# Kernel tuning notes

Hardware: AMD Instinct MI355X
Metric: run time of the kernel (lower is better)

Reference implementation:

```python
import jax, jax.numpy as jnp
import numpy as np

B, NF, S, L, H, MID, KS, NC, DENSE = 16, 8, 16, 256, 128, 32, 8, 10, 512
COEFF = 0.1
BN_EPS = 1e-5


def _normalize(x):
    return x / jnp.maximum(jnp.linalg.norm(x, axis=-1, keepdims=True), 1e-12)


def _sparsemax(z):
    # sparsemax over last axis (Martins & Astudillo 2016)
    zs = jnp.flip(jnp.sort(z, axis=-1), axis=-1)
    k = jnp.arange(1, z.shape[-1] + 1, dtype=z.dtype)
    cum = jnp.cumsum(zs, axis=-1)
    support = (1.0 + k * zs) > cum
    ksup = jnp.sum(support, axis=-1, keepdims=True)
    tau = (jnp.take_along_axis(cum, ksup - 1, axis=-1) - 1.0) / ksup.astype(z.dtype)
    return jnp.maximum(z - tau, 0.0)


def _bn_ncl(x, g, b, m, v):  # eval-mode BatchNorm1d on [N, C, L]
    return g[None, :, None] * (x - m[None, :, None]) * jax.lax.rsqrt(v[None, :, None] + BN_EPS) + b[None, :, None]


def _bn_nc(x, g, b, m, v):  # eval-mode BatchNorm1d on [N, C]
    return g * (x - m) * jax.lax.rsqrt(v + BN_EPS) + b


def _conv(x, w, pad):
    return jax.lax.conv_general_dilated(x, w, (1,), [(pad, pad)], dimension_numbers=('NCH', 'OIH', 'NCH'))


def _maxpool2(x):  # MaxPool1d(kernel=2, stride=2, padding=1): -inf padded
    return jax.lax.reduce_window(x, -jnp.inf, jax.lax.max, (1, 1, 2), (1, 1, 2), ((0, 0), (0, 0), (1, 1)))


def _cnn(x, cw1, bn1, cw2, bn2, cw3, bn3):
    x = _maxpool2(jax.nn.relu(_bn_ncl(_conv(x, cw1, KS // 2), *bn1)))
    x = _maxpool2(jax.nn.relu(_bn_ncl(_conv(x, cw2, 4), *bn2)))
    x = _maxpool2(jax.nn.relu(_bn_ncl(_conv(x, cw3, 4), *bn3)))
    return jnp.mean(x, axis=-1)  # AdaptiveAvgPool1d(1) -> [N, H]


def _alpha_beta(x, cw1, bn1, cw2, bn2, cw3, bn3, Wq, bq, Wk, bk, Wv, bv):
    b = x.shape[0]
    xf = jnp.transpose(x, (1, 0, 2, 3)).reshape(NF, b * S, 1, L)
    rep = jax.vmap(_cnn)(xf, cw1, bn1, cw2, bn2, cw3, bn3)  # [F, B*S, H]
    rep = rep.reshape(NF, b, S, H)
    Q = jax.nn.elu(rep @ Wq + bq)
    K = jax.nn.leaky_relu(rep @ Wk + bk)
    V = jax.nn.leaky_relu(rep @ Wv + bv)
    # mean_t(Q @ K^T) == Q @ mean_t(K); then scale by sqrt(d_k)
    scores = jnp.einsum('fbsh,fbh->fbs', Q, jnp.mean(K, axis=2)) / jnp.sqrt(jnp.float32(H))
    intra_aw = _sparsemax(scores)                             # [F, B, S]
    Z = _normalize(jnp.einsum('fbs,fbsh->fbh', intra_aw, V))  # [F, B, H]
    Kn = _normalize(rep)
    inter_scores = jnp.einsum('ibh,fbsh->ifbs', Z, Kn)        # cosine scores (Z already unit-norm)
    inter_aw = _sparsemax(inter_scores)                       # [I, F, B, S]
    U = jnp.einsum('ifbs,fbsh->ibh', inter_aw, rep) / NF      # mean over feature axis f
    Hc = _normalize(jnp.concatenate([Z, U], axis=-1))         # [F, B, 2H]
    feat = jnp.transpose(Hc, (1, 0, 2)).reshape(b, NF * 2 * H)
    return feat, intra_aw, inter_aw


def _forward(src_x, src_y, tgt_x, cw1, bn1_g, bn1_b, bn1_m, bn1_v, cw2, bn2_g, bn2_b, bn2_m, bn2_v, cw3, bn3_g, bn3_b, bn3_m, bn3_v, Wq, bq, Wk, bk, Wv, bv, bnc1_g, bnc1_b, bnc1_m, bnc1_v, W1, b1, bnc2_g, bnc2_b, bnc2_m, bnc2_v, W2, b2):
    bn1 = (bn1_g, bn1_b, bn1_m, bn1_v)
    bn2 = (bn2_g, bn2_b, bn2_m, bn2_v)
    bn3 = (bn3_g, bn3_b, bn3_m, bn3_v)
    sf, sa, sb = _alpha_beta(src_x, cw1, bn1, cw2, bn2, cw3, bn3, Wq, bq, Wk, bk, Wv, bv)
    _, ta, tb = _alpha_beta(tgt_x, cw1, bn1, cw2, bn2, cw3, bn3, Wq, bq, Wk, bk, Wv, bv)
    h = _bn_nc(sf, bnc1_g, bnc1_b, bnc1_m, bnc1_v) @ W1 + b1
    h = jax.nn.leaky_relu(_bn_nc(h, bnc2_g, bnc2_b, bnc2_m, bnc2_v))
    y_pred = jax.nn.softmax(h @ W2 + b2, axis=-1)
    # MMD domain losses (detached in original via torch.tensor(list))
    da = jnp.mean(sa - ta, axis=-2)                           # [F, S]
    loss_a = COEFF * jnp.mean(jnp.linalg.norm(da, axis=-1))
    db = jnp.mean(sb - tb, axis=-2)                           # [I, F, S]
    loss_b = COEFF * jnp.mean(jnp.sqrt(jnp.sum(db * db, axis=(1, 2))))
    dom = jax.lax.stop_gradient(loss_a + loss_b)
    # CrossEntropyLoss applied to already-softmaxed preds, as in source
    logp = jax.nn.log_softmax(y_pred, axis=-1)
    ce = -jnp.mean(logp[jnp.arange(y_pred.shape[0]), src_y])
    return y_pred, ce + dom


def setup_inputs() -> dict:
    ks = jax.random.split(jax.random.key(0), 40)
    rn = lambda i, sh, s=1.0: s * jax.random.normal(ks[i], sh, dtype=jnp.float32)
    ru = lambda i, sh, lo, hi: jax.random.uniform(ks[i], sh, jnp.float32, lo, hi)
    return {
        'src_x': rn(0, (B, NF, S, L)),
        'src_y': jax.random.randint(ks[1], (B,), 0, NC),
        'tgt_x': rn(2, (B, NF, S, L)),
        'cw1': rn(3, (NF, MID, 1, KS), 0.1),
        'bn1_g': ru(4, (NF, MID), 0.75, 1.25), 'bn1_b': rn(5, (NF, MID), 0.1),
        'bn1_m': rn(6, (NF, MID), 0.1), 'bn1_v': ru(7, (NF, MID), 0.5, 1.5),
        'cw2': rn(8, (NF, 2 * MID, MID, 8), 0.05),
        'bn2_g': ru(9, (NF, 2 * MID), 0.75, 1.25), 'bn2_b': rn(10, (NF, 2 * MID), 0.1),
        'bn2_m': rn(11, (NF, 2 * MID), 0.1), 'bn2_v': ru(12, (NF, 2 * MID), 0.5, 1.5),
        'cw3': rn(13, (NF, H, 2 * MID, 8), 0.05),
        'bn3_g': ru(14, (NF, H), 0.75, 1.25), 'bn3_b': rn(15, (NF, H), 0.1),
        'bn3_m': rn(16, (NF, H), 0.1), 'bn3_v': ru(17, (NF, H), 0.5, 1.5),
        'Wq': rn(18, (H, H), 0.05), 'bq': rn(19, (H,), 0.02),
        'Wk': rn(20, (H, H), 0.05), 'bk': rn(21, (H,), 0.02),
        'Wv': rn(22, (H, H), 0.05), 'bv': rn(23, (H,), 0.02),
        'bnc1_g': ru(24, (NF * 2 * H,), 0.75, 1.25), 'bnc1_b': rn(25, (NF * 2 * H,), 0.1),
        'bnc1_m': rn(26, (NF * 2 * H,), 0.1), 'bnc1_v': ru(27, (NF * 2 * H,), 0.5, 1.5),
        'W1': rn(28, (NF * 2 * H, DENSE), 0.03), 'b1': rn(29, (DENSE,), 0.02),
        'bnc2_g': ru(30, (DENSE,), 0.75, 1.25), 'bnc2_b': rn(31, (DENSE,), 0.1),
        'bnc2_m': rn(32, (DENSE,), 0.1), 'bnc2_v': ru(33, (DENSE,), 0.5, 1.5),
        'W2': rn(34, (DENSE, NC), 0.05), 'b2': rn(35, (NC,), 0.02),
    }


def reference(src_x, src_y, tgt_x, cw1, bn1_g, bn1_b, bn1_m, bn1_v, cw2, bn2_g, bn2_b, bn2_m, bn2_v, cw3, bn3_g, bn3_b, bn3_m, bn3_v, Wq, bq, Wk, bk, Wv, bv, bnc1_g, bnc1_b, bnc1_m, bnc1_v, W1, b1, bnc2_g, bnc2_b, bnc2_m, bnc2_v, W2, b2):
    return _forward(src_x, src_y, tgt_x, cw1, bn1_g, bn1_b, bn1_m, bn1_v, cw2, bn2_g, bn2_b, bn2_m, bn2_v, cw3, bn3_g, bn3_b, bn3_m, bn3_v, Wq, bq, Wk, bk, Wv, bv, bnc1_g, bnc1_b, bnc1_m, bnc1_v, W1, b1, bnc2_g, bnc2_b, bnc2_m, bnc2_v, W2, b2)
```

## Files before the change

### kernel.cpp

```cpp
#include <hip/hip_runtime.h>

typedef unsigned short u16;
typedef unsigned int u32;
typedef __attribute__((ext_vector_type(8))) short bfrag;
typedef __attribute__((ext_vector_type(4))) float ffrag;

__device__ __forceinline__ float lrelu(float x) { return x >= 0.f ? x : 0.01f * x; }
__device__ __forceinline__ float eluf(float x)  { return x > 0.f ? x : expm1f(x); }
__device__ __forceinline__ u16 f2bf(float f) {
    u32 x = __float_as_uint(f);
    return (u16)((x + 0x7fffu + ((x >> 16) & 1u)) >> 16);
}
__device__ __forceinline__ u16 f2bt(float f) {
    return (u16)(__float_as_uint(f) >> 16);
}
__device__ __forceinline__ float bf2f(u16 u) {
    return __uint_as_float(((u32)u) << 16);
}

__device__ void sparsemax16(const float* z, float* out) {
    float zs[16];
    for (int i = 0; i < 16; ++i) zs[i] = z[i];
    for (int i = 1; i < 16; ++i) {
        float key = zs[i]; int j = i - 1;
        while (j >= 0 && zs[j] < key) { zs[j + 1] = zs[j]; --j; }
        zs[j + 1] = key;
    }
    float cum[16];
    cum[0] = zs[0];
    for (int i = 1; i < 16; ++i) cum[i] = cum[i - 1] + zs[i];
    int ksup = 0;
    for (int k = 1; k <= 16; ++k)
        if (1.0f + (float)k * zs[k - 1] > cum[k - 1]) ksup++;
    if (ksup < 1) ksup = 1;
    float tau = (cum[ksup - 1] - 1.0f) / (float)ksup;
    for (int i = 0; i < 16; ++i) out[i] = fmaxf(z[i] - tau, 0.0f);
}

__global__ __launch_bounds__(256) void k_wprep(
    const float* __restrict__ w2, const float* __restrict__ w3,
    const float* __restrict__ Wq, const float* __restrict__ Wk,
    const float* __restrict__ Wv,
    u16* __restrict__ wpk2, u16* __restrict__ wpk3, u16* __restrict__ wqkv)
{
    int i = blockIdx.x * 256 + threadIdx.x;
    if (i < 131072) {
        int j = i & 7, L = (i >> 3) & 63, kc = (i >> 9) & 7, nt = (i >> 12) & 3, f = i >> 14;
        int co = nt * 16 + (L & 15);
        int ci = ((L >> 4) << 3) + j;
        wpk2[i] = f2bf(w2[(((size_t)f * 64 + co) * 32 + ci) * 8 + kc]);
    } else if (i < 131072 + 524288) {
        int i2 = i - 131072;
        int j = i2 & 7, L = (i2 >> 3) & 63, kc = (i2 >> 9) & 15, nt = (i2 >> 13) & 7, f = i2 >> 16;
        int co = nt * 16 + (L & 15);
        int ci = ((kc & 1) << 5) + ((L >> 4) << 3) + j;
        wpk3[i2] = f2bf(w3[(((size_t)f * 128 + co) * 64 + ci) * 8 + (kc >> 1)]);
    } else if (i < 131072 + 524288 + 49152) {
        int j2 = i - 655360;
        int proj = j2 >> 14, idx = j2 & 16383;
        int jj = idx & 7, L = (idx >> 3) & 63, kc = (idx >> 9) & 3, nt = idx >> 11;
        int n = nt * 16 + (L & 15);
        int k = kc * 32 + ((L >> 4) << 3) + jj;
        const float* W = proj == 0 ? Wq : (proj == 1 ? Wk : Wv);
        wqkv[j2] = f2bf(W[k * 128 + n]);
    }
}

#define S1T_STRIDE 40
#define S2T_STRIDE 72
#define RB2_STRIDE 68
#define RB3_STRIDE 140
#define RB_OFF 6336
#define SMEM_U16 (RB_OFF + 67 * RB3_STRIDE)

__global__ __launch_bounds__(256) void k_cnn(
    const float* __restrict__ xs, const float* __restrict__ xt,
    const float* __restrict__ w1, const float* __restrict__ g1, const float* __restrict__ b1,
    const float* __restrict__ m1, const float* __restrict__ v1,
    const float* __restrict__ g2, const float* __restrict__ b2,
    const float* __restrict__ m2, const float* __restrict__ v2,
    const float* __restrict__ g3, const float* __restrict__ b3,
    const float* __restrict__ m3, const float* __restrict__ v3,
    const u16* __restrict__ wpk2, const u16* __restrict__ wpk3,
    float* __restrict__ rep)
{
    __shared__ __align__(16) u16 smem[SMEM_U16];
    float* xin = (float*)(smem + RB_OFF);

    int tid = threadIdx.x, blk = blockIdx.x;
    int pass = blk >> 11, f = (blk >> 8) & 7, n = blk & 255;
    int bb = n >> 4, ss = n & 15;
    int lane = tid & 63, w = tid >> 6;
    const float* x = pass ? xt : xs;
    float* rep_p = rep + (size_t)pass * 262144;

    {
        u32* z = (u32*)smem;
        for (int i = tid; i < 3168; i += 256) z[i] = 0;
        for (int i = tid; i < 264; i += 256) xin[i] = 0.f;
    }
    __syncthreads();
    {
        const float* xr = x + (((size_t)bb * 8 + f) * 16 + ss) * 256;
        for (int i = tid; i < 256; i += 256) xin[i + 4] = xr[i];
    }
    __syncthreads();

    if (tid < 208) {
        int cc = tid & 7, jc = tid >> 3;
        int co0 = cc * 4, j0 = jc * 5;
        float wr[4][8];
        for (int c = 0; c < 4; ++c) {
            const float4* q = reinterpret_cast<const float4*>(w1 + ((size_t)f * 32 + co0 + c) * 8);
            float4 a = q[0], bq = q[1];
            wr[c][0] = a.x; wr[c][1] = a.y; wr[c][2] = a.z; wr[c][3] = a.w;
            wr[c][4] = bq.x; wr[c][5] = bq.y; wr[c][6] = bq.z; wr[c][7] = bq.w;
        }
        int px[10];
        for (int i = 0; i < 10; ++i) {
            int p = 2 * j0 - 1 + i;
            px[i] = p < 0 ? 0 : (p > 256 ? 256 : p);
        }
        float acc[4][10];
        for (int c = 0; c < 4; ++c) for (int i = 0; i < 10; ++i) acc[c][i] = 0.f;
        for (int k = 0; k < 8; ++k) {
            float xv[10];
            for (int i = 0; i < 10; ++i) xv[i] = xin[px[i] + k];
            for (int c = 0; c < 4; ++c)
                for (int i = 0; i < 10; ++i) acc[c][i] += wr[c][k] * xv[i];
        }
        for (int c = 0; c < 4; ++c) {
            int co = co0 + c;
            float sc = g1[f * 32 + co] * rsqrtf(v1[f * 32 + co] + 1e-5f);
            float sh = b1[f * 32 + co] - m1[f * 32 + co] * sc;
            for (int jj = 0; jj < 5; ++jj) {
                int j = j0 + jj;
                if (j < 129) {
                    float a0 = fmaxf(acc[c][2 * jj] * sc + sh, 0.f);
                    float a1 = fmaxf(acc[c][2 * jj + 1] * sc + sh, 0.f);
                    smem[(j + 4) * S1T_STRIDE + co] = f2bt(fmaxf(a0, a1));
                }
            }
        }
    }
    __syncthreads();

    {
        int nt = w;
        bfrag B2[8];
        const bfrag* gB = reinterpret_cast<const bfrag*>(wpk2);
        for (int kc = 0; kc < 8; ++kc)
            B2[kc] = gB[(((size_t)f * 4 + nt) * 8 + kc) * 64 + lane];
        int co = nt * 16 + (lane & 15);
        float sc = g2[f * 64 + co] * rsqrtf(v2[f * 64 + co] + 1e-5f);
        float sh = b2[f * 64 + co] - m2[f * 64 + co] * sc;
        int arow = lane & 15, ci0 = (lane >> 4) << 3;
        for (int mt = 0; mt < 9; ++mt) {
            ffrag C = {0.f, 0.f, 0.f, 0.f};
            int rb = mt * 16 + arow;
            for (int kc = 0; kc < 8; ++kc) {
                bfrag A = *reinterpret_cast<const bfrag*>(&smem[(rb + kc) * S1T_STRIDE + ci0]);
                C = __builtin_amdgcn_mfma_f32_16x16x32_bf16(A, B2[kc], C, 0, 0, 0);
            }
            int p0 = mt * 16 + ((lane >> 4) << 2);
            for (int r = 0; r < 4; ++r) {
                int p = p0 + r;
                if (p < 130)
                    smem[RB_OFF + p * RB2_STRIDE + co] = f2bt(fmaxf(C[r] * sc + sh, 0.f));
            }
        }
    }
    __syncthreads();

    {
        u32* z = (u32*)smem;
        for (int i = tid; i < 3168; i += 256) z[i] = 0;
    }
    __syncthreads();

    for (int e = tid; e < 66 * 64; e += 256) {
        int j = e >> 6, ci = e & 63;
        float vmax;
        if (j == 0) {
            vmax = bf2f(smem[RB_OFF + 0 * RB2_STRIDE + ci]);
        } else if (j == 65) {
            vmax = bf2f(smem[RB_OFF + 129 * RB2_STRIDE + ci]);
        } else {
            float a0 = bf2f(smem[RB_OFF + (2 * j - 1) * RB2_STRIDE + ci]);
            float a1 = bf2f(smem[RB_OFF + (2 * j) * RB2_STRIDE + ci]);
            vmax = fmaxf(a0, a1);
        }
        smem[(j + 4) * S2T_STRIDE + ci] = f2bt(vmax);
    }
    __syncthreads();

    for (int t = 0; t < 2; ++t) {
        int nt = w * 2 + t;
        bfrag B3[16];
        const bfrag* gB = reinterpret_cast<const bfrag*>(wpk3);
        for (int kc = 0; kc < 16; ++kc)
            B3[kc] = gB[(((size_t)f * 8 + nt) * 16 + kc) * 64 + lane];
        int co = nt * 16 + (lane & 15);
        float sc = g3[f * 128 + co] * rsqrtf(v3[f * 128 + co] + 1e-5f);
        float sh = b3[f * 128 + co] - m3[f * 128 + co] * sc;
        int arow = lane & 15, q8 = (lane >> 4) << 3;
        for (int mt = 0; mt < 5; ++mt) {
            ffrag C = {0.f, 0.f, 0.f, 0.f};
            int rb = mt * 16 + arow;
            for (int kc = 0; kc < 16; ++kc) {
                int row = rb + (kc >> 1);
                int ci0 = ((kc & 1) << 5) + q8;
                bfrag A = *reinterpret_cast<const bfrag*>(&smem[row * S2T_STRIDE + ci0]);
                C = __builtin_amdgcn_mfma_f32_16x16x32_bf16(A, B3[kc], C, 0, 0, 0);
            }
            int p0 = mt * 16 + ((lane >> 4) << 2);
            for (int r = 0; r < 4; ++r) {
                int p = p0 + r;
                if (p < 67)
                    smem[RB_OFF + p * RB3_STRIDE + co] = f2bt(fmaxf(C[r] * sc + sh, 0.f));
            }
        }
    }
    __syncthreads();

    if (tid < 128) {
        int co = tid;
        float sum = bf2f(smem[RB_OFF + 0 * RB3_STRIDE + co]);
        for (int j = 1; j < 34; ++j) {
            float a0 = bf2f(smem[RB_OFF + (2 * j - 1) * RB3_STRIDE + co]);
            float a1 = bf2f(smem[RB_OFF + (2 * j) * RB3_STRIDE + co]);
            sum += fmaxf(a0, a1);
        }
        rep_p[(((size_t)f * 256) + n) * 128 + co] = sum * (1.0f / 34.0f);
    }
}

__global__ __launch_bounds__(256) void k_attn1(
    const float* __restrict__ rep, const u16* __restrict__ wqkv,
    const float* __restrict__ bq, const float* __restrict__ bk,
    const float* __restrict__ bv,
    float* __restrict__ Zn, float* __restrict__ rninv, float* __restrict__ iaw)
{
    __shared__ __align__(16) u16 repbf[16 * 136];
    __shared__ float KmL[128], ZL[128], awL[16], scoresL[16], r2L[16];
    __shared__ float spart[4][4][4];
    __shared__ float redL[4];
    int tid = threadIdx.x;
    int pass = blockIdx.x >> 7, f = (blockIdx.x >> 4) & 7, b = blockIdx.x & 15;
    const float* rp = rep + (size_t)pass * 262144 + ((size_t)f * 256 + b * 16) * 128;
    float* Zn_p = Zn + (size_t)pass * 16384;
    float* rninv_p = rninv + (size_t)pass * 2048;
    float* iaw_p = iaw + (size_t)pass * 2048;

    {
        int s = tid >> 4, i = tid & 15, h0 = i * 8;
        const float4* q4 = reinterpret_cast<const float4*>(rp + s * 128 + h0);
        float4 a = q4[0], c = q4[1];
        float p2 = a.x*a.x + a.y*a.y + a.z*a.z + a.w*a.w
                 + c.x*c.x + c.y*c.y + c.z*c.z + c.w*c.w;
        bfrag pk;
        pk[0] = (short)f2bt(a.x); pk[1] = (short)f2bt(a.y);
        pk[2] = (short)f2bt(a.z); pk[3] = (short)f2bt(a.w);
        pk[4] = (short)f2bt(c.x); pk[5] = (short)f2bt(c.y);
        pk[6] = (short)f2bt(c.z); pk[7] = (short)f2bt(c.w);
        *reinterpret_cast<bfrag*>(&repbf[s * 136 + h0]) = pk;
        p2 += __shfl_xor(p2, 1); p2 += __shfl_xor(p2, 2);
        p2 += __shfl_xor(p2, 4); p2 += __shfl_xor(p2, 8);
        if (i == 0) r2L[s] = p2;
    }
    __syncthreads();

    int lane = tid & 63, w = tid >> 6, arow = lane & 15, q = lane >> 4;
    bfrag A[4];
    for (int kc = 0; kc < 4; ++kc)
        A[kc] = *reinterpret_cast<const bfrag*>(&repbf[arow * 136 + kc * 32 + q * 8]);

    float qv[2][4], vvv[2][4];
    int colv[2];
    const bfrag* BB = reinterpret_cast<const bfrag*>(wqkv);
    for (int t = 0; t < 2; ++t) {
        int nt = w * 2 + t;
        ffrag cq = {0.f,0.f,0.f,0.f}, ck = {0.f,0.f,0.f,0.f}, cv = {0.f,0.f,0.f,0.f};
        for (int kc = 0; kc < 4; ++kc) {
            int fi = (nt * 4 + kc) * 64 + lane;
            bfrag Bq = BB[fi];
            bfrag Bk = BB[2048 + fi];
            bfrag Bv = BB[4096 + fi];
            cq = __builtin_amdgcn_mfma_f32_16x16x32_bf16(A[kc], Bq, cq, 0, 0, 0);
            ck = __builtin_amdgcn_mfma_f32_16x16x32_bf16(A[kc], Bk, ck, 0, 0, 0);
            cv = __builtin_amdgcn_mfma_f32_16x16x32_bf16(A[kc], Bv, cv, 0, 0, 0);
        }
        int col = nt * 16 + arow;
        colv[t] = col;
        float bqc = bq[col], bkc = bk[col], bvc = bv[col];
        float kpt = 0.f;
        for (int r = 0; r < 4; ++r) {
            qv[t][r] = eluf(cq[r] + bqc);
            vvv[t][r] = lrelu(cv[r] + bvc);
            kpt += lrelu(ck[r] + bkc);
        }
        kpt += __shfl_xor(kpt, 16);
        kpt += __shfl_xor(kpt, 32);
        if (q == 0) KmL[col] = kpt * (1.f / 16.f);
    }
    __syncthreads();

    {
        float km0 = KmL[colv[0]], km1 = KmL[colv[1]];
        float ps[4];
        for (int r = 0; r < 4; ++r) {
            float v = qv[0][r] * km0 + qv[1][r] * km1;
            v += __shfl_xor(v, 1); v += __shfl_xor(v, 2);
            v += __shfl_xor(v, 4); v += __shfl_xor(v, 8);
            ps[r] = v;
        }
        if (arow == 0)
            for (int r = 0; r < 4; ++r) spart[w][q][r] = ps[r];
    }
    __syncthreads();
    if (tid < 16) {
        int qq = tid >> 2, rr = tid & 3;
        float sc = spart[0][qq][rr] + spart[1][qq][rr] + spart[2][qq][rr] + spart[3][qq][rr];
        scoresL[tid] = sc * 0.08838834764831845f;
        rninv_p[f * 256 + b * 16 + tid] = 1.f / fmaxf(sqrtf(r2L[tid]), 1e-12f);
    }
    __syncthreads();
    if (tid == 0) sparsemax16(scoresL, awL);
    __syncthreads();
    if (tid < 16) iaw_p[f * 256 + b * 16 + tid] = awL[tid];

    for (int t = 0; t < 2; ++t) {
        float zp = 0.f;
        for (int r = 0; r < 4; ++r) zp += awL[q * 4 + r] * vvv[t][r];
        zp += __shfl_xor(zp, 16);
        zp += __shfl_xor(zp, 32);
        if (q == 0) ZL[colv[t]] = zp;
    }
    __syncthreads();
    if (tid < 128) {
        float z = ZL[tid];
        float v = z * z;
        v += __shfl_xor(v, 1); v += __shfl_xor(v, 2); v += __shfl_xor(v, 4);
        v += __shfl_xor(v, 8); v += __shfl_xor(v, 16); v += __shfl_xor(v, 32);
        if (lane == 0) redL[w] = v;
    }
    __syncthreads();
    if (tid == 0) redL[2] = 1.f / fmaxf(sqrtf(redL[0] + redL[1]), 1e-12f);
    __syncthreads();
    if (tid < 128)
        Zn_p[((size_t)f * 16 + b) * 128 + tid] = ZL[tid] * redL[2];
}

__global__ __launch_bounds__(256) void k_attn2(
    const float* __restrict__ rep, const float* __restrict__ Zn,
    const float* __restrict__ rninv, float* __restrict__ ibw,
    const float* __restrict__ g, const float* __restrict__ bb,
    const float* __restrict__ mm, const float* __restrict__ vv,
    float* __restrict__ featbn)
{
    __shared__ float ZnL[1024], sc[1024], UL[1024], nrm[8];
    int tid = threadIdx.x;
    int pass = blockIdx.x >> 4, b = blockIdx.x & 15;
    const float* rep_p = rep + (size_t)pass * 262144;
    const float* Zn_p = Zn + (size_t)pass * 16384;
    const float* rninv_p = rninv + (size_t)pass * 2048;
    float* ibw_p = ibw + (size_t)pass * 16384;

    for (int i = tid; i < 1024; i += 256) {
        int ii = i >> 7, h = i & 127;
        ZnL[i] = Zn_p[((size_t)ii * 16 + b) * 128 + h];
    }
    if (tid < 8) nrm[tid] = 0.f;
    __syncthreads();

    for (int e = tid; e < 1024; e += 256) {
        int i = e >> 7, f = (e >> 4) & 7, s = e & 15;
        const float* rr = rep_p + ((size_t)f * 256 + b * 16 + s) * 128;
        float a = 0.f;
        for (int h = 0; h < 128; ++h) a += ZnL[i * 128 + h] * rr[h];
        sc[(i * 8 + f) * 16 + s] = a * rninv_p[f * 256 + b * 16 + s];
    }
    __syncthreads();
    if (tid < 64) {
        int i = tid >> 3, f = tid & 7;
        float aw[16];
        sparsemax16(&sc[(i * 8 + f) * 16], aw);
        for (int s = 0; s < 16; ++s) {
            sc[(i * 8 + f) * 16 + s] = aw[s];
            ibw_p[(((size_t)i * 8 + f) * 16 + b) * 16 + s] = aw[s];
        }
    }
    __syncthreads();
    if (pass == 0) {
        for (int e = tid; e < 1024; e += 256) {
            int i = e >> 7, h = e & 127;
            float u = 0.f;
            for (int f = 0; f < 8; ++f) {
                const float* rr = rep_p + ((size_t)f * 256 + b * 16) * 128 + h;
                const float* aa = &sc[(i * 8 + f) * 16];
                for (int s = 0; s < 16; ++s) u += aa[s] * rr[s * 128];
            }
            UL[e] = u * 0.125f;
        }
        __syncthreads();
        for (int e = tid; e < 1024; e += 256) {
            int f = e >> 7;
            float zz = ZnL[e], uu = UL[e];
            atomicAdd(&nrm[f], zz * zz + uu * uu);
        }
        __syncthreads();
        for (int e = tid; e < 2048; e += 256) {
            int f = e >> 8, d = e & 255;
            float inv = 1.f / fmaxf(sqrtf(nrm[f]), 1e-12f);
            float val = (d < 128 ? ZnL[f * 128 + d] : UL[f * 128 + d - 128]) * inv;
            float scv = g[e] * rsqrtf(vv[e] + 1e-5f);
            featbn[b * 2048 + e] = (val - mm[e]) * scv + bb[e];
        }
    }
}

__global__ __launch_bounds__(256) void k_head1(
    const float* __restrict__ featbn,
    const float* __restrict__ W1, const float* __restrict__ b1,
    const float* __restrict__ g2, const float* __restrict__ bb2,
    const float* __restrict__ mm2, const float* __restrict__ vv2,
    float* __restrict__ h2ws)
{
    __shared__ float featL[2048];
    __shared__ float part[8][32];
    int tid = threadIdx.x, blk = blockIdx.x;
    int b = blk >> 4, cc = blk & 15;
    for (int i = tid; i < 2048; i += 256) featL[i] = featbn[b * 2048 + i];
    __syncthreads();
    int ci = tid & 31, ks = tid >> 5;
    int col = cc * 32 + ci;
    const float* wcol = W1 + (size_t)(ks * 256) * 512 + col;
    const float* fl = featL + ks * 256;
    float a = 0.f;
    for (int c = 0; c < 256; ++c) a += fl[c] * wcol[(size_t)c * 512];
    part[ks][ci] = a;
    __syncthreads();
    if (tid < 32) {
        int colw = cc * 32 + tid;
        float s = b1[colw];
        for (int k2 = 0; k2 < 8; ++k2) s += part[k2][tid];
        float scv = g2[colw] * rsqrtf(vv2[colw] + 1e-5f);
        float val = (s - mm2[colw]) * scv + bb2[colw];
        h2ws[b * 512 + colw] = lrelu(val);
    }
}

__global__ __launch_bounds__(256) void k_tail(
    const float* __restrict__ h2ws,
    const float* __restrict__ W2, const float* __restrict__ b2,
    const float* __restrict__ sa, const float* __restrict__ ta,
    const float* __restrict__ sb, const float* __restrict__ tb,
    const int* __restrict__ sy, float* __restrict__ dout)
{
    __shared__ float h2L[8192];
    __shared__ float lgL[160], ypL[160];
    __shared__ float sA[8], sB[8];
    int tid = threadIdx.x;
    for (int i = tid; i < 8192; i += 256) h2L[i] = h2ws[i];
    if (tid < 8) { sA[tid] = 0.f; sB[tid] = 0.f; }
    __syncthreads();
    if (tid < 160) {
        int b = tid / 10, j = tid - b * 10;
        float a = b2[j];
        const float* h = h2L + b * 512;
        for (int c = 0; c < 512; ++c) a += h[c] * W2[c * 10 + j];
        lgL[tid] = a;
    }
    __syncthreads();
    if (tid < 16) {
        int b = tid;
        float mx = lgL[b * 10];
        for (int j = 1; j < 10; ++j) mx = fmaxf(mx, lgL[b * 10 + j]);
        float sum = 0.f, ex[10];
        for (int j = 0; j < 10; ++j) { ex[j] = expf(lgL[b * 10 + j] - mx); sum += ex[j]; }
        for (int j = 0; j < 10; ++j) {
            float p = ex[j] / sum;
            ypL[b * 10 + j] = p;
            dout[b * 10 + j] = p;
        }
    }
    __syncthreads();
    if (tid < 128) {
        int f = tid >> 4, s = tid & 15;
        float d = 0.f;
        for (int b = 0; b < 16; ++b) d += sa[f * 256 + b * 16 + s] - ta[f * 256 + b * 16 + s];
        d *= (1.f / 16.f);
        atomicAdd(&sA[f], d * d);
    }
    for (int e = tid; e < 1024; e += 256) {
        int i = e >> 7, f = (e >> 4) & 7, s = e & 15;
        float d = 0.f;
        int base = ((i * 8 + f) * 16) * 16 + s;
        for (int b = 0; b < 16; ++b) d += sb[base + b * 16] - tb[base + b * 16];
        d *= (1.f / 16.f);
        atomicAdd(&sB[i], d * d);
    }
    __syncthreads();
    if (tid == 0) {
        float la = 0.f, lb = 0.f;
        for (int f = 0; f < 8; ++f) la += sqrtf(sA[f]);
        for (int i = 0; i < 8; ++i) lb += sqrtf(sB[i]);
        la *= 0.1f / 8.f;
        lb *= 0.1f / 8.f;
        float ce = 0.f;
        for (int b = 0; b < 16; ++b) {
            const float* y = ypL + b * 10;
            float mx = y[0];
            for (int j = 1; j < 10; ++j) mx = fmaxf(mx, y[j]);
            float sum = 0.f;
            for (int j = 0; j < 10; ++j) sum += expf(y[j] - mx);
            float lse = mx + logf(sum);
            ce += lse - y[sy[b]];
        }
        ce *= (1.f / 16.f);
        dout[160] = ce + la + lb;
    }
}

extern "C" void kernel_launch(void* const* d_in, const int* in_sizes, int n_in,
                              void* d_out, int out_size, void* d_ws, size_t ws_size,
                              hipStream_t stream) {
    (void)in_sizes; (void)n_in; (void)out_size; (void)ws_size;
    const float* src_x = (const float*)d_in[0];
    const int*   src_y = (const int*)d_in[1];
    const float* tgt_x = (const float*)d_in[2];
    const float *cw1 = (const float*)d_in[3], *bn1g = (const float*)d_in[4],
                *bn1b = (const float*)d_in[5], *bn1m = (const float*)d_in[6],
                *bn1v = (const float*)d_in[7];
    const float *cw2 = (const float*)d_in[8], *bn2g = (const float*)d_in[9],
                *bn2b = (const float*)d_in[10], *bn2m = (const float*)d_in[11],
                *bn2v = (const float*)d_in[12];
    const float *cw3 = (const float*)d_in[13], *bn3g = (const float*)d_in[14],
                *bn3b = (const float*)d_in[15], *bn3m = (const float*)d_in[16],
                *bn3v = (const float*)d_in[17];
    const float *Wq = (const float*)d_in[18], *bq = (const float*)d_in[19],
                *Wk = (const float*)d_in[20], *bk = (const float*)d_in[21],
                *Wv = (const float*)d_in[22], *bv = (const float*)d_in[23];
    const float *bc1g = (const float*)d_in[24], *bc1b = (const float*)d_in[25],
                *bc1m = (const float*)d_in[26], *bc1v = (const float*)d_in[27];
    const float *W1 = (const float*)d_in[28], *b1 = (const float*)d_in[29];
    const float *bc2g = (const float*)d_in[30], *bc2b = (const float*)d_in[31],
                *bc2m = (const float*)d_in[32], *bc2v = (const float*)d_in[33];
    const float *W2 = (const float*)d_in[34], *b2 = (const float*)d_in[35];

    float* ws = (float*)d_ws;
    size_t o = 0;
    float* rep    = ws + o; o += (size_t)2 * 262144;
    float* Zn     = ws + o; o += (size_t)2 * 16384;
    float* rninv  = ws + o; o += (size_t)2 * 2048;
    float* ia     = ws + o; o += (size_t)2 * 2048;
    float* ib     = ws + o; o += (size_t)2 * 16384;
    float* featbn = ws + o; o += (size_t)16 * 2048;
    float* h2ws   = ws + o; o += (size_t)16 * 512;
    u16* wpk2 = (u16*)(ws + o); o += 65536;
    u16* wpk3 = (u16*)(ws + o); o += 262144;
    u16* wqkv = (u16*)(ws + o); o += 24576;

    k_wprep<<<2752, 256, 0, stream>>>(cw2, cw3, Wq, Wk, Wv, wpk2, wpk3, wqkv);
    k_cnn<<<4096, 256, 0, stream>>>(src_x, tgt_x,
        cw1, bn1g, bn1b, bn1m, bn1v,
        bn2g, bn2b, bn2m, bn2v,
        bn3g, bn3b, bn3m, bn3v,
        wpk2, wpk3, rep);
    k_attn1<<<256, 256, 0, stream>>>(rep, wqkv, bq, bk, bv, Zn, rninv, ia);
    k_attn2<<<32, 256, 0, stream>>>(rep, Zn, rninv, ib, bc1g, bc1b, bc1m, bc1v, featbn);
    k_head1<<<256, 256, 0, stream>>>(featbn, W1, b1, bc2g, bc2b, bc2m, bc2v, h2ws);
    k_tail<<<1, 256, 0, stream>>>(h2ws, W2, b2, ia, ia + 2048, ib, ib + 16384,
                                  src_y, (float*)d_out);
}
```

Before: 333.2 us.

## Fuse attention kernels into one per-batch kernel with rep staged in LDS

Merges k_attn1 and k_attn2 into one kernel of 32 blocks. Each block loads its batch's rep slice (all 8 features) into shared memory once, then computes intra-attention for each feature in a serial loop and goes straight on to inter-attention from LDS. This drops one launch and the global round trips for Zn and rninv, but cuts parallelism from 256 blocks to 32 and uses about 80KB of LDS per block. k_head1 is also reworked to split K into 32 slices with float4 loads of W1 columns.

Result: slower. 405.6 us (+21.8%).

```diff
diff --git a/kernel.cpp b/kernel.cpp
--- a/kernel.cpp
+++ b/kernel.cpp
@@ -235,158 +235,151 @@
     }
 }
 
-__global__ __launch_bounds__(256) void k_attn1(
+__global__ __launch_bounds__(256) void k_attn(
     const float* __restrict__ rep, const u16* __restrict__ wqkv,
     const float* __restrict__ bq, const float* __restrict__ bk,
     const float* __restrict__ bv,
-    float* __restrict__ Zn, float* __restrict__ rninv, float* __restrict__ iaw)
-{
-    __shared__ __align__(16) u16 repbf[16 * 136];
-    __shared__ float KmL[128], ZL[128], awL[16], scoresL[16], r2L[16];
-    __shared__ float spart[4][4][4];
-    __shared__ float redL[4];
-    int tid = threadIdx.x;
-    int pass = blockIdx.x >> 7, f = (blockIdx.x >> 4) & 7, b = blockIdx.x & 15;
-    const float* rp = rep + (size_t)pass * 262144 + ((size_t)f * 256 + b * 16) * 128;
-    float* Zn_p = Zn + (size_t)pass * 16384;
-    float* rninv_p = rninv + (size_t)pass * 2048;
-    float* iaw_p = iaw + (size_t)pass * 2048;
-
-    {
-        int s = tid >> 4, i = tid & 15, h0 = i * 8;
-        const float4* q4 = reinterpret_cast<const float4*>(rp + s * 128 + h0);
-        float4 a = q4[0], c = q4[1];
-        float p2 = a.x*a.x + a.y*a.y + a.z*a.z + a.w*a.w
-                 + c.x*c.x + c.y*c.y + c.z*c.z + c.w*c.w;
-        bfrag pk;
-        pk[0] = (short)f2bt(a.x); pk[1] = (short)f2bt(a.y);
-        pk[2] = (short)f2bt(a.z); pk[3] = (short)f2bt(a.w);
-        pk[4] = (short)f2bt(c.x); pk[5] = (short)f2bt(c.y);
-        pk[6] = (short)f2bt(c.z); pk[7] = (short)f2bt(c.w);
-        *reinterpret_cast<bfrag*>(&repbf[s * 136 + h0]) = pk;
-        p2 += __shfl_xor(p2, 1); p2 += __shfl_xor(p2, 2);
-        p2 += __shfl_xor(p2, 4); p2 += __shfl_xor(p2, 8);
-        if (i == 0) r2L[s] = p2;
-    }
-    __syncthreads();
-
-    int lane = tid & 63, w = tid >> 6, arow = lane & 15, q = lane >> 4;
-    bfrag A[4];
-    for (int kc = 0; kc < 4; ++kc)
-        A[kc] = *reinterpret_cast<const bfrag*>(&repbf[arow * 136 + kc * 32 + q * 8]);
-
-    float qv[2][4], vvv[2][4];
-    int colv[2];
-    const bfrag* BB = reinterpret_cast<const bfrag*>(wqkv);
-    for (int t = 0; t < 2; ++t) {
-        int nt = w * 2 + t;
-        ffrag cq = {0.f,0.f,0.f,0.f}, ck = {0.f,0.f,0.f,0.f}, cv = {0.f,0.f,0.f,0.f};
-        for (int kc = 0; kc < 4; ++kc) {
-            int fi = (nt * 4 + kc) * 64 + lane;
-            bfrag Bq = BB[fi];
-            bfrag Bk = BB[2048 + fi];
-            bfrag Bv = BB[4096 + fi];
-            cq = __builtin_amdgcn_mfma_f32_16x16x32_bf16(A[kc], Bq, cq, 0, 0, 0);
-            ck = __builtin_amdgcn_mfma_f32_16x16x32_bf16(A[kc], Bk, ck, 0, 0, 0);
-            cv = __builtin_amdgcn_mfma_f32_16x16x32_bf16(A[kc], Bv, cv, 0, 0, 0);
-        }
-        int col = nt * 16 + arow;
-        colv[t] = col;
-        float bqc = bq[col], bkc = bk[col], bvc = bv[col];
-        float kpt = 0.f;
-        for (int r = 0; r < 4; ++r) {
-            qv[t][r] = eluf(cq[r] + bqc);
-            vvv[t][r] = lrelu(cv[r] + bvc);
-            kpt += lrelu(ck[r] + bkc);
-        }
-        kpt += __shfl_xor(kpt, 16);
-        kpt += __shfl_xor(kpt, 32);
-        if (q == 0) KmL[col] = kpt * (1.f / 16.f);
-    }
-    __syncthreads();
-
-    {
-        float km0 = KmL[colv[0]], km1 = KmL[colv[1]];
-        float ps[4];
-        for (int r = 0; r < 4; ++r) {
-            float v = qv[0][r] * km0 + qv[1][r] * km1;
-            v += __shfl_xor(v, 1); v += __shfl_xor(v, 2);
-            v += __shfl_xor(v, 4); v += __shfl_xor(v, 8);
-            ps[r] = v;
-        }
-        if (arow == 0)
-            for (int r = 0; r < 4; ++r) spart[w][q][r] = ps[r];
-    }
-    __syncthreads();
-    if (tid < 16) {
-        int qq = tid >> 2, rr = tid & 3;
-        float sc = spart[0][qq][rr] + spart[1][qq][rr] + spart[2][qq][rr] + spart[3][qq][rr];
-        scoresL[tid] = sc * 0.08838834764831845f;
-        rninv_p[f * 256 + b * 16 + tid] = 1.f / fmaxf(sqrtf(r2L[tid]), 1e-12f);
-    }
-    __syncthreads();
-    if (tid == 0) sparsemax16(scoresL, awL);
-    __syncthreads();
-    if (tid < 16) iaw_p[f * 256 + b * 16 + tid] = awL[tid];
-
-    for (int t = 0; t < 2; ++t) {
-        float zp = 0.f;
-        for (int r = 0; r < 4; ++r) zp += awL[q * 4 + r] * vvv[t][r];
-        zp += __shfl_xor(zp, 16);
-        zp += __shfl_xor(zp, 32);
-        if (q == 0) ZL[colv[t]] = zp;
-    }
-    __syncthreads();
-    if (tid < 128) {
-        float z = ZL[tid];
-        float v = z * z;
-        v += __shfl_xor(v, 1); v += __shfl_xor(v, 2); v += __shfl_xor(v, 4);
-        v += __shfl_xor(v, 8); v += __shfl_xor(v, 16); v += __shfl_xor(v, 32);
-        if (lane == 0) redL[w] = v;
-    }
-    __syncthreads();
-    if (tid == 0) redL[2] = 1.f / fmaxf(sqrtf(redL[0] + redL[1]), 1e-12f);
-    __syncthreads();
-    if (tid < 128)
-        Zn_p[((size_t)f * 16 + b) * 128 + tid] = ZL[tid] * redL[2];
-}
-
-__global__ __launch_bounds__(256) void k_attn2(
-    const float* __restrict__ rep, const float* __restrict__ Zn,
-    const float* __restrict__ rninv, float* __restrict__ ibw,
+    float* __restrict__ iaw, float* __restrict__ ibw,
     const float* __restrict__ g, const float* __restrict__ bb,
     const float* __restrict__ mm, const float* __restrict__ vv,
     float* __restrict__ featbn)
 {
-    __shared__ float ZnL[1024], sc[1024], UL[1024], nrm[8];
+    __shared__ float repL[16384];
+    __shared__ __align__(16) u16 repbf[16 * 136];
+    __shared__ float ZnL[1024];
+    __shared__ float scL[1024], UL[1024];
+    __shared__ float rinvL[128], KmL[128], ZL[128];
+    __shared__ float awL[16], scoresL[16];
+    __shared__ float spart[4][4][4], redL[4], nrm[8];
     int tid = threadIdx.x;
     int pass = blockIdx.x >> 4, b = blockIdx.x & 15;
     const float* rep_p = rep + (size_t)pass * 262144;
-    const float* Zn_p = Zn + (size_t)pass * 16384;
-    const float* rninv_p = rninv + (size_t)pass * 2048;
+    float* iaw_p = iaw + (size_t)pass * 2048;
     float* ibw_p = ibw + (size_t)pass * 16384;
-
-    for (int i = tid; i < 1024; i += 256) {
-        int ii = i >> 7, h = i & 127;
-        ZnL[i] = Zn_p[((size_t)ii * 16 + b) * 128 + h];
+    int lane = tid & 63, w = tid >> 6, arow = lane & 15, q = lane >> 4;
+
+    for (int f = 0; f < 8; ++f) {
+        const float4* src = reinterpret_cast<const float4*>(
+            rep_p + ((size_t)f * 256 + b * 16) * 128);
+        float4* dst = reinterpret_cast<float4*>(repL + f * 2048);
+        for (int i = tid; i < 512; i += 256) dst[i] = src[i];
     }
     if (tid < 8) nrm[tid] = 0.f;
     __syncthreads();
+
+    if (tid < 128) {
+        const float* r = repL + tid * 128;
+        float s = 0.f;
+        for (int h = 0; h < 128; ++h) { float v = r[h]; s += v * v; }
+        rinvL[tid] = 1.f / fmaxf(sqrtf(s), 1e-12f);
+    }
+    __syncthreads();
+
+    const bfrag* BB = reinterpret_cast<const bfrag*>(wqkv);
+    for (int f = 0; f < 8; ++f) {
+        {
+            int s = tid >> 4, i = tid & 15, h0 = i * 8;
+            const float* r = repL + (f * 16 + s) * 128 + h0;
+            bfrag pk;
+            for (int j = 0; j < 8; ++j) pk[j] = (short)f2bt(r[j]);
+            *reinterpret_cast<bfrag*>(&repbf[s * 136 + h0]) = pk;
+        }
+        __syncthreads();
+
+        bfrag A[4];
+        for (int kc = 0; kc < 4; ++kc)
+            A[kc] = *reinterpret_cast<const bfrag*>(&repbf[arow * 136 + kc * 32 + q * 8]);
+
+        float qv[2][4], vvv[2][4];
+        int colv[2];
+        for (int t = 0; t < 2; ++t) {
+            int nt = w * 2 + t;
+            ffrag cq = {0.f,0.f,0.f,0.f}, ck = {0.f,0.f,0.f,0.f}, cv = {0.f,0.f,0.f,0.f};
+            for (int kc = 0; kc < 4; ++kc) {
+                int fi = (nt * 4 + kc) * 64 + lane;
+                bfrag Bq = BB[fi];
+                bfrag Bk = BB[2048 + fi];
+                bfrag Bv = BB[4096 + fi];
+                cq = __builtin_amdgcn_mfma_f32_16x16x32_bf16(A[kc], Bq, cq, 0, 0, 0);
+                ck = __builtin_amdgcn_mfma_f32_16x16x32_bf16(A[kc], Bk, ck, 0, 0, 0);
+                cv = __builtin_amdgcn_mfma_f32_16x16x32_bf16(A[kc], Bv, cv, 0, 0, 0);
+            }
+            int col = nt * 16 + arow;
+            colv[t] = col;
+            float bqc = bq[col], bkc = bk[col], bvc = bv[col];
+            float kpt = 0.f;
+            for (int r = 0; r < 4; ++r) {
+                qv[t][r] = eluf(cq[r] + bqc);
+                vvv[t][r] = lrelu(cv[r] + bvc);
+                kpt += lrelu(ck[r] + bkc);
+            }
+            kpt += __shfl_xor(kpt, 16);
+            kpt += __shfl_xor(kpt, 32);
+            if (q == 0) KmL[col] = kpt * (1.f / 16.f);
+        }
+        __syncthreads();
+
+        {
+            float km0 = KmL[colv[0]], km1 = KmL[colv[1]];
+            float ps[4];
+            for (int r = 0; r < 4; ++r) {
+                float v = qv[0][r] * km0 + qv[1][r] * km1;
+                v += __shfl_xor(v, 1); v += __shfl_xor(v, 2);
+                v += __shfl_xor(v, 4); v += __shfl_xor(v, 8);
+                ps[r] = v;
+            }
+            if (arow == 0)
+                for (int r = 0; r < 4; ++r) spart[w][q][r] = ps[r];
+        }
+        __syncthreads();
+        if (tid < 16) {
+            int qq = tid >> 2, rr = tid & 3;
+            float sc = spart[0][qq][rr] + spart[1][qq][rr]
+                     + spart[2][qq][rr] + spart[3][qq][rr];
+            scoresL[tid] = sc * 0.08838834764831845f;
+        }
+        __syncthreads();
+        if (tid == 0) sparsemax16(scoresL, awL);
+        __syncthreads();
+        if (tid < 16) iaw_p[f * 256 + b * 16 + tid] = awL[tid];
+
+        for (int t = 0; t < 2; ++t) {
+            float zp = 0.f;
+            for (int r = 0; r < 4; ++r) zp += awL[q * 4 + r] * vvv[t][r];
+            zp += __shfl_xor(zp, 16);
+            zp += __shfl_xor(zp, 32);
+            if (q == 0) ZL[colv[t]] = zp;
+        }
+        __syncthreads();
+        if (tid < 128) {
+            float z = ZL[tid];
+            float v = z * z;
+            v += __shfl_xor(v, 1); v += __shfl_xor(v, 2); v += __shfl_xor(v, 4);
+            v += __shfl_xor(v, 8); v += __shfl_xor(v, 16); v += __shfl_xor(v, 32);
+            if (lane == 0) redL[w] = v;
+        }
+        __syncthreads();
+        if (tid == 0) redL[2] = 1.f / fmaxf(sqrtf(redL[0] + redL[1]), 1e-12f);
+        __syncthreads();
+        if (tid < 128) ZnL[f * 128 + tid] = ZL[tid] * redL[2];
+        __syncthreads();
+    }
 
     for (int e = tid; e < 1024; e += 256) {
         int i = e >> 7, f = (e >> 4) & 7, s = e & 15;
-        const float* rr = rep_p + ((size_t)f * 256 + b * 16 + s) * 128;
+        const float* zr = ZnL + i * 128;
+        const float* rr = repL + (f * 16 + s) * 128;
         float a = 0.f;
-        for (int h = 0; h < 128; ++h) a += ZnL[i * 128 + h] * rr[h];
-        sc[(i * 8 + f) * 16 + s] = a * rninv_p[f * 256 + b * 16 + s];
+        for (int h = 0; h < 128; ++h) a += zr[h] * rr[h];
+        scL[(i * 8 + f) * 16 + s] = a * rinvL[f * 16 + s];
     }
     __syncthreads();
     if (tid < 64) {
         int i = tid >> 3, f = tid & 7;
         float aw[16];
-        sparsemax16(&sc[(i * 8 + f) * 16], aw);
+        sparsemax16(&scL[(i * 8 + f) * 16], aw);
         for (int s = 0; s < 16; ++s) {
-            sc[(i * 8 + f) * 16 + s] = aw[s];
+            scL[(i * 8 + f) * 16 + s] = aw[s];
             ibw_p[(((size_t)i * 8 + f) * 16 + b) * 16 + s] = aw[s];
         }
     }
@@ -396,8 +389,8 @@
             int i = e >> 7, h = e & 127;
             float u = 0.f;
             for (int f = 0; f < 8; ++f) {
-                const float* rr = rep_p + ((size_t)f * 256 + b * 16) * 128 + h;
-                const float* aa = &sc[(i * 8 + f) * 16];
+                const float* rr = repL + f * 2048 + h;
+                const float* aa = &scL[(i * 8 + f) * 16];
                 for (int s = 0; s < 16; ++s) u += aa[s] * rr[s * 128];
             }
             UL[e] = u * 0.125f;
@@ -427,23 +420,35 @@
     float* __restrict__ h2ws)
 {
     __shared__ float featL[2048];
-    __shared__ float part[8][32];
+    __shared__ float part[32][32];
     int tid = threadIdx.x, blk = blockIdx.x;
     int b = blk >> 4, cc = blk & 15;
-    for (int i = tid; i < 2048; i += 256) featL[i] = featbn[b * 2048 + i];
-    __syncthreads();
-    int ci = tid & 31, ks = tid >> 5;
-    int col = cc * 32 + ci;
-    const float* wcol = W1 + (size_t)(ks * 256) * 512 + col;
-    const float* fl = featL + ks * 256;
-    float a = 0.f;
-    for (int c = 0; c < 256; ++c) a += fl[c] * wcol[(size_t)c * 512];
-    part[ks][ci] = a;
+    {
+        const float4* src = reinterpret_cast<const float4*>(featbn + b * 2048);
+        float4* dst = reinterpret_cast<float4*>(featL);
+        for (int i = tid; i < 512; i += 256) dst[i] = src[i];
+    }
+    __syncthreads();
+    int ks = tid >> 3, cg = tid & 7;
+    int col0 = cc * 32 + cg * 4;
+    float4 acc = {0.f, 0.f, 0.f, 0.f};
+    const float* fl = featL + ks * 64;
+    for (int c = 0; c < 64; ++c) {
+        int k = ks * 64 + c;
+        float4 wv = *reinterpret_cast<const float4*>(W1 + (size_t)k * 512 + col0);
+        float fv = fl[c];
+        acc.x += fv * wv.x; acc.y += fv * wv.y;
+        acc.z += fv * wv.z; acc.w += fv * wv.w;
+    }
+    part[ks][cg * 4 + 0] = acc.x;
+    part[ks][cg * 4 + 1] = acc.y;
+    part[ks][cg * 4 + 2] = acc.z;
+    part[ks][cg * 4 + 3] = acc.w;
     __syncthreads();
     if (tid < 32) {
         int colw = cc * 32 + tid;
         float s = b1[colw];
-        for (int k2 = 0; k2 < 8; ++k2) s += part[k2][tid];
+        for (int k2 = 0; k2 < 32; ++k2) s += part[k2][tid];
         float scv = g2[colw] * rsqrtf(vv2[colw] + 1e-5f);
         float val = (s - mm2[colw]) * scv + bb2[colw];
         h2ws[b * 512 + colw] = lrelu(val);
@@ -551,8 +556,6 @@
     float* ws = (float*)d_ws;
     size_t o = 0;
     float* rep    = ws + o; o += (size_t)2 * 262144;
-    float* Zn     = ws + o; o += (size_t)2 * 16384;
-    float* rninv  = ws + o; o += (size_t)2 * 2048;
     float* ia     = ws + o; o += (size_t)2 * 2048;
     float* ib     = ws + o; o += (size_t)2 * 16384;
     float* featbn = ws + o; o += (size_t)16 * 2048;
@@ -567,8 +570,8 @@
         bn2g, bn2b, bn2m, bn2v,
         bn3g, bn3b, bn3m, bn3v,
         wpk2, wpk3, rep);
-    k_attn1<<<256, 256, 0, stream>>>(rep, wqkv, bq, bk, bv, Zn, rninv, ia);
-    k_attn2<<<32, 256, 0, stream>>>(rep, Zn, rninv, ib, bc1g, bc1b, bc1m, bc1v, featbn);
+    k_attn<<<32, 256, 0, stream>>>(rep, wqkv, bq, bk, bv, ia, ib,
+                                   bc1g, bc1b, bc1m, bc1v, featbn);
     k_head1<<<256, 256, 0, stream>>>(featbn, W1, b1, bc2g, bc2b, bc2m, bc2v, h2ws);
     k_tail<<<1, 256, 0, stream>>>(h2ws, W2, b2, ia, ia + 2048, ib, ib + 16384,
                                   src_y, (float*)d_out);
```

## Split inter-attention kernel across query features and vectorize head matmul

Applied to the files above, without the earlier changes.

k_attn2 now runs 256 blocks instead of 32, one per (pass, batch, query feature). Each block stages the batch's rep slice into shared memory with float4 loads and computes a single query's scores, sparsemax, aggregation and norm using wave shuffles in place of shared atomics. k_head1 has each thread load float4 columns of W1 over a 64-wide K slice with a 32-way partial reduction, which coalesces the weight reads. The cost is that the rep slice is reloaded redundantly by 8 blocks and each block uses 64KB of LDS.

Result: faster. 314.9 us (-5.5%).

```diff
diff --git a/kernel.cpp b/kernel.cpp
--- a/kernel.cpp
+++ b/kernel.cpp
@@ -358,61 +358,66 @@
     const float* __restrict__ mm, const float* __restrict__ vv,
     float* __restrict__ featbn)
 {
-    __shared__ float ZnL[1024], sc[1024], UL[1024], nrm[8];
-    int tid = threadIdx.x;
-    int pass = blockIdx.x >> 4, b = blockIdx.x & 15;
+    __shared__ float repL[16384];
+    __shared__ float ZiL[128], scores[128], UL[128];
+    __shared__ float awLf[8][16];
+    __shared__ float redL[2];
+    int tid = threadIdx.x, blk = blockIdx.x;
+    int pass = blk >> 7, b = (blk >> 3) & 15, i = blk & 7;
     const float* rep_p = rep + (size_t)pass * 262144;
-    const float* Zn_p = Zn + (size_t)pass * 16384;
-    const float* rninv_p = rninv + (size_t)pass * 2048;
-    float* ibw_p = ibw + (size_t)pass * 16384;
-
-    for (int i = tid; i < 1024; i += 256) {
-        int ii = i >> 7, h = i & 127;
-        ZnL[i] = Zn_p[((size_t)ii * 16 + b) * 128 + h];
-    }
-    if (tid < 8) nrm[tid] = 0.f;
-    __syncthreads();
-
-    for (int e = tid; e < 1024; e += 256) {
-        int i = e >> 7, f = (e >> 4) & 7, s = e & 15;
-        const float* rr = rep_p + ((size_t)f * 256 + b * 16 + s) * 128;
+
+    for (int f = 0; f < 8; ++f) {
+        const float4* src = reinterpret_cast<const float4*>(
+            rep_p + ((size_t)f * 256 + b * 16) * 128);
+        float4* dst = reinterpret_cast<float4*>(repL + f * 2048);
+        for (int t = tid; t < 512; t += 256) dst[t] = src[t];
+    }
+    if (tid < 128) ZiL[tid] = Zn[(size_t)pass * 16384 + ((size_t)i * 16 + b) * 128 + tid];
+    __syncthreads();
+
+    if (tid < 128) {
+        int f = tid >> 4, s = tid & 15;
+        const float* rr = repL + tid * 128;
         float a = 0.f;
-        for (int h = 0; h < 128; ++h) a += ZnL[i * 128 + h] * rr[h];
-        sc[(i * 8 + f) * 16 + s] = a * rninv_p[f * 256 + b * 16 + s];
-    }
-    __syncthreads();
-    if (tid < 64) {
-        int i = tid >> 3, f = tid & 7;
+        for (int h = 0; h < 128; ++h) a += ZiL[h] * rr[h];
+        scores[tid] = a * rninv[(size_t)pass * 2048 + f * 256 + b * 16 + s];
+    }
+    __syncthreads();
+    if (tid < 8) {
         float aw[16];
-        sparsemax16(&sc[(i * 8 + f) * 16], aw);
-        for (int s = 0; s < 16; ++s) {
-            sc[(i * 8 + f) * 16 + s] = aw[s];
-            ibw_p[(((size_t)i * 8 + f) * 16 + b) * 16 + s] = aw[s];
-        }
-    }
-    __syncthreads();
+        sparsemax16(&scores[tid * 16], aw);
+        for (int s = 0; s < 16; ++s) awLf[tid][s] = aw[s];
+    }
+    __syncthreads();
+    if (tid < 128) {
+        int f = tid >> 4, s = tid & 15;
+        ibw[(size_t)pass * 16384 + (((size_t)i * 8 + f) * 16 + b) * 16 + s] = awLf[f][s];
+    }
     if (pass == 0) {
-        for (int e = tid; e < 1024; e += 256) {
-            int i = e >> 7, h = e & 127;
+        if (tid < 128) {
+            int h = tid;
             float u = 0.f;
             for (int f = 0; f < 8; ++f) {
-                const float* rr = rep_p + ((size_t)f * 256 + b * 16) * 128 + h;
-                const float* aa = &sc[(i * 8 + f) * 16];
+                const float* rr = repL + f * 2048 + h;
+                const float* aa = awLf[f];
                 for (int s = 0; s < 16; ++s) u += aa[s] * rr[s * 128];
             }
-            UL[e] = u * 0.125f;
+            UL[h] = u * 0.125f;
         }
         __syncthreads();
-        for (int e = tid; e < 1024; e += 256) {
-            int f = e >> 7;
-            float zz = ZnL[e], uu = UL[e];
-            atomicAdd(&nrm[f], zz * zz + uu * uu);
+        if (tid < 128) {
+            int lane = tid & 63, w = tid >> 6;
+            float v = ZiL[tid] * ZiL[tid] + UL[tid] * UL[tid];
+            v += __shfl_xor(v, 1); v += __shfl_xor(v, 2); v += __shfl_xor(v, 4);
+            v += __shfl_xor(v, 8); v += __shfl_xor(v, 16); v += __shfl_xor(v, 32);
+            if (lane == 0) redL[w] = v;
         }
         __syncthreads();
-        for (int e = tid; e < 2048; e += 256) {
-            int f = e >> 8, d = e & 255;
-            float inv = 1.f / fmaxf(sqrtf(nrm[f]), 1e-12f);
-            float val = (d < 128 ? ZnL[f * 128 + d] : UL[f * 128 + d - 128]) * inv;
+        if (tid < 256) {
+            float inv = 1.f / fmaxf(sqrtf(redL[0] + redL[1]), 1e-12f);
+            int d = tid;
+            int e = i * 256 + d;
+            float val = (d < 128 ? ZiL[d] : UL[d - 128]) * inv;
             float scv = g[e] * rsqrtf(vv[e] + 1e-5f);
             featbn[b * 2048 + e] = (val - mm[e]) * scv + bb[e];
         }
@@ -427,23 +432,35 @@
     float* __restrict__ h2ws)
 {
     __shared__ float featL[2048];
-    __shared__ float part[8][32];
+    __shared__ float part[32][32];
     int tid = threadIdx.x, blk = blockIdx.x;
     int b = blk >> 4, cc = blk & 15;
-    for (int i = tid; i < 2048; i += 256) featL[i] = featbn[b * 2048 + i];
-    __syncthreads();
-    int ci = tid & 31, ks = tid >> 5;
-    int col = cc * 32 + ci;
-    const float* wcol = W1 + (size_t)(ks * 256) * 512 + col;
-    const float* fl = featL + ks * 256;
-    float a = 0.f;
-    for (int c = 0; c < 256; ++c) a += fl[c] * wcol[(size_t)c * 512];
-    part[ks][ci] = a;
+    {
+        const float4* src = reinterpret_cast<const float4*>(featbn + b * 2048);
+        float4* dst = reinterpret_cast<float4*>(featL);
+        for (int i = tid; i < 512; i += 256) dst[i] = src[i];
+    }
+    __syncthreads();
+    int ks = tid >> 3, cg = tid & 7;
+    int col0 = cc * 32 + cg * 4;
+    float4 acc = {0.f, 0.f, 0.f, 0.f};
+    const float* fl = featL + ks * 64;
+    for (int c = 0; c < 64; ++c) {
+        int k = ks * 64 + c;
+        float4 wv = *reinterpret_cast<const float4*>(W1 + (size_t)k * 512 + col0);
+        float fv = fl[c];
+        acc.x += fv * wv.x; acc.y += fv * wv.y;
+        acc.z += fv * wv.z; acc.w += fv * wv.w;
+    }
+    part[ks][cg * 4 + 0] = acc.x;
+    part[ks][cg * 4 + 1] = acc.y;
+    part[ks][cg * 4 + 2] = acc.z;
+    part[ks][cg * 4 + 3] = acc.w;
     __syncthreads();
     if (tid < 32) {
         int colw = cc * 32 + tid;
         float s = b1[colw];
-        for (int k2 = 0; k2 < 8; ++k2) s += part[k2][tid];
+        for (int k2 = 0; k2 < 32; ++k2) s += part[k2][tid];
         float scv = g2[colw] * rsqrtf(vv2[colw] + 1e-5f);
         float val = (s - mm2[colw]) * scv + bb2[colw];
         h2ws[b * 512 + colw] = lrelu(val);
@@ -568,7 +585,7 @@
         bn3g, bn3b, bn3m, bn3v,
         wpk2, wpk3, rep);
     k_attn1<<<256, 256, 0, stream>>>(rep, wqkv, bq, bk, bv, Zn, rninv, ia);
-    k_attn2<<<32, 256, 0, stream>>>(rep, Zn, rninv, ib, bc1g, bc1b, bc1m, bc1v, featbn);
+    k_attn2<<<256, 256, 0, stream>>>(rep, Zn, rninv, ib, bc1g, bc1b, bc1m, bc1v, featbn);
     k_head1<<<256, 256, 0, stream>>>(featbn, W1, b1, bc2g, bc2b, bc2m, bc2v, h2ws);
     k_tail<<<1, 256, 0, stream>>>(h2ws, W2, b2, ia, ia + 2048, ib, ib + 16384,
                                   src_y, (float*)d_out);
```
